# Kernel tuning notes

Hardware: AMD Instinct MI355X
Metric: run time of the kernel (lower is better)

Reference implementation:

```python
import jax, jax.numpy as jnp
import numpy as np
from jax import lax

B, S, P, H = 256, 336, 96, 512


def setup_inputs() -> dict:
    key = jax.random.key(0)
    ks = jax.random.split(key, 18)
    def n(k, shape, s=0.05):
        return jax.random.normal(k, shape, dtype=jnp.float32) * s
    return {
        "x": jax.random.normal(ks[0], (B, S, 7), dtype=jnp.float32),
        "lin_enc_w": n(ks[1], (H, 3)), "lin_enc_b": n(ks[2], (H,)),
        "quat_enc_w": n(ks[3], (H, 4)), "quat_enc_b": n(ks[4], (H,)),
        "lin_wih": n(ks[5], (4 * H, H)), "lin_whh": n(ks[6], (4 * H, H)),
        "lin_bih": n(ks[7], (4 * H,)), "lin_bhh": n(ks[8], (4 * H,)),
        "quat_wih": n(ks[9], (4 * H, H)), "quat_whh": n(ks[10], (4 * H, H)),
        "quat_bih": n(ks[11], (4 * H,)), "quat_bhh": n(ks[12], (4 * H,)),
        "lin_dec_w": n(ks[13], (3, H)), "lin_dec_b": n(ks[14], (3,)),
        "quat_dec_w": n(ks[15], (4, H)), "quat_dec_b": n(ks[16], (4,)),
        "pred_len": P,
    }


def _lstm_cell(carry, xt, Wih, Whh, bih, bhh):
    # PyTorch gate order: i, f, g, o
    h, c = carry
    g = xt @ Wih.T + bih + h @ Whh.T + bhh  # [B, 4H]
    i, f, gg, o = jnp.split(g, 4, axis=-1)
    c = jax.nn.sigmoid(f) * c + jax.nn.sigmoid(i) * jnp.tanh(gg)
    h = jax.nn.sigmoid(o) * jnp.tanh(c)
    return (h, c), h


def _branch(xc, We, be, Wih, Whh, bih, bhh, Wd, bd, pred_len):
    e = xc @ We.T + be  # [B, S, H]
    Bn, _, Hn = e.shape
    cell = lambda carry, xt: _lstm_cell(carry, xt, Wih, Whh, bih, bhh)
    z = jnp.zeros((Bn, Hn), e.dtype)
    (h, _), outs = lax.scan(cell, (z, z), jnp.swapaxes(e, 0, 1))  # outs: [S, B, H]
    # Each prediction step feeds h as input to the LSTM with ZERO initial state
    # (the original code does not pass (h, c) back in).
    def pred_step(h, _):
        (hn, _), _ = cell((jnp.zeros_like(h), jnp.zeros_like(h)), h)
        return hn, hn
    _, preds = lax.scan(pred_step, h, None, length=pred_len)  # [P, B, H]
    seq = jnp.concatenate([outs, preds], axis=0)[1:]  # drop first step -> [S+P-1, B, H]
    return jnp.swapaxes(seq, 0, 1) @ Wd.T + bd


def reference(x, lin_enc_w, lin_enc_b, quat_enc_w, quat_enc_b,
              lin_wih, lin_whh, lin_bih, lin_bhh,
              quat_wih, quat_whh, quat_bih, quat_bhh,
              lin_dec_w, lin_dec_b, quat_dec_w, quat_dec_b, pred_len):
    lx = _branch(x[:, :, :3], lin_enc_w, lin_enc_b, lin_wih, lin_whh,
                 lin_bih, lin_bhh, lin_dec_w, lin_dec_b, pred_len)
    rx = _branch(x[:, :, 3:], quat_enc_w, quat_enc_b, quat_wih, quat_whh,
                 quat_bih, quat_bhh, quat_dec_w, quat_dec_b, pred_len)
    return jnp.concatenate([lx, rx], axis=2)  # [B, S+P-1, 7]
```

## Files before the change

kernel.cpp:

```cpp
#include <hip/hip_runtime.h>

#define BB 256
#define SS 336
#define HH 512
#define NT 431
#define NU 432

typedef __attribute__((ext_vector_type(8))) short bf16x8;
typedef __attribute__((ext_vector_type(16))) float f32x16;
typedef __attribute__((ext_vector_type(4))) int i32x4;


__device__ inline unsigned short f2bf(float f) {
    unsigned int u = __float_as_uint(f);
    unsigned int r = (u + 0x7fffu + ((u >> 16) & 1u)) >> 16;
    return (unsigned short)r;
}
__device__ inline float sigm(float x) { return 1.f / (1.f + __expf(-x)); }
__device__ inline float tanh_(float x) { return 2.f / (1.f + __expf(-2.f * x)) - 1.f; }

__device__ inline i32x4 llc_load_b128(const i32x4* p) {
    i32x4 r;
    asm volatile("global_load_dwordx4 %0, %1, off sc0 sc1" : "=v"(r) : "v"(p));
    return r;
}
__device__ inline void llc_store_b128(i32x4* p, i32x4 v) {
    asm volatile("global_store_dwordx4 %0, %1, off sc0 sc1" :: "v"(p), "v"(v) : "memory");
}
__device__ inline void vm_drain() { asm volatile("s_waitcnt vmcnt(0)" ::: "memory"); }

__global__ void k_wfrag(const float* __restrict__ w0, const float* __restrict__ w1,
                        const float* __restrict__ w2, const float* __restrict__ w3,
                        unsigned short* __restrict__ wfrag) {
    int idx = blockIdx.x * 256 + threadIdx.x;
    int mat = idx >> 17;
    int t = idx & 131071;
    int lane = t & 63;
    int kb = (t >> 6) & 31;
    int csub = (t >> 11) & 1;
    int cg = t >> 12;
    const float* W = mat == 0 ? w0 : (mat == 1 ? w1 : (mat == 2 ? w2 : w3));
    int n_local = csub * 32 + (lane & 31);
    int n = (n_local >> 4) * 512 + cg * 16 + (n_local & 15);
    int k0 = kb * 16 + (lane >> 5) * 8;
    const float* src = W + n * 512 + k0;
    unsigned short us[8];
#pragma unroll
    for (int j = 0; j < 8; ++j) us[j] = f2bf(src[j]);
    i32x4 v;
    v.x = us[0] | (us[1] << 16); v.y = us[2] | (us[3] << 16);
    v.z = us[4] | (us[5] << 16); v.w = us[6] | (us[7] << 16);
    ((i32x4*)wfrag)[idx] = v;
}

__global__ void k_mbias(const float* __restrict__ lin_wih, const float* __restrict__ quat_wih,
                        const float* __restrict__ lin_enc_w, const float* __restrict__ quat_enc_w,
                        const float* __restrict__ lin_enc_b, const float* __restrict__ quat_enc_b,
                        const float* __restrict__ lin_bih, const float* __restrict__ lin_bhh,
                        const float* __restrict__ quat_bih, const float* __restrict__ quat_bhh,
                        float* __restrict__ M, float* __restrict__ bE, float* __restrict__ bP) {
    int gid = blockIdx.x * 256 + threadIdx.x;
    int branch = gid >> 11;
    int n = gid & 2047;
    int nf = 3 + branch;
    const float* Wih = branch ? quat_wih : lin_wih;
    const float* We  = branch ? quat_enc_w : lin_enc_w;
    const float* be  = branch ? quat_enc_b : lin_enc_b;
    const float* bih = branch ? quat_bih : lin_bih;
    const float* bhh = branch ? quat_bhh : lin_bhh;
    float m[4] = {0.f, 0.f, 0.f, 0.f};
    float bs = 0.f;
    for (int j = 0; j < 512; ++j) {
        float w = Wih[n * 512 + j];
#pragma unroll
        for (int kf = 0; kf < 4; ++kf)
            if (kf < nf) m[kf] += w * We[j * nf + kf];
        bs += w * be[j];
    }
    float* Mp = M + (branch * 2048 + n) * 4;
#pragma unroll
    for (int kf = 0; kf < 4; ++kf) Mp[kf] = m[kf];
    bE[branch * 2048 + n] = bs + bih[n] + bhh[n];
    bP[branch * 2048 + n] = bih[n] + bhh[n];
}

__global__ void k_zero(i32x4* __restrict__ p) {
    int idx = blockIdx.x * 256 + threadIdx.x;
    p[idx] = i32x4{0, 0, 0, 0};
}

__global__ __launch_bounds__(256, 1) void k_persist(
    const float* __restrict__ x,
    const unsigned short* __restrict__ wfrag,
    const float* __restrict__ M, const float* __restrict__ bE, const float* __restrict__ bP,
    const float* __restrict__ lin_dec_w, const float* __restrict__ quat_dec_w,
    const float* __restrict__ lin_dec_b, const float* __restrict__ quat_dec_b,
    unsigned short* __restrict__ hbuf,
    float* __restrict__ out,
    unsigned int* __restrict__ bar) {
    __shared__ i32x4 lds_a[4096];
    __shared__ float g_lds[64 * 65];
    __shared__ float h_tile[64 * 17];
    __shared__ float mE[256];
    __shared__ float bEs[64];
    __shared__ float bPs[64];

    const int tid = threadIdx.x;
    const int lane = tid & 63;
    const int wv = tid >> 6;
    const int rsub = wv & 1, csub = wv >> 1;
    const int blk = blockIdx.x;
    const int branch = blk >> 7;
    const int rg = (blk >> 5) & 3;
    const int cg = blk & 31;
    const int group = blk >> 5;
    const int nf = 3 + branch;
    const int row = tid & 63;
    const int jbase = tid >> 6;
    const int b = rg * 64 + row;

    {
        int gate = tid >> 6, jj = (tid >> 2) & 15, kf = tid & 3;
        mE[tid] = M[(size_t)(branch * 2048 + gate * 512 + cg * 16 + jj) * 4 + kf];
    }
    if (tid < 64) {
        int gate = tid >> 4, jj = tid & 15;
        bEs[tid] = bE[branch * 2048 + gate * 512 + cg * 16 + jj];
        bPs[tid] = bP[branch * 2048 + gate * 512 + cg * 16 + jj];
    }

    const int dr   = lane & 1;
    const int dd   = (lane >> 1) & 3;
    const int dseg = lane >> 3;
    const int drow = cg * 2 + dr;
    const bool dvalid = dd < nf;
    const float* dwp = (branch ? quat_dec_w : lin_dec_w) + dd * 512;
    const float dbias = dvalid ? (branch ? quat_dec_b : lin_dec_b)[dd] : 0.f;

    const i32x4* BpE = (const i32x4*)wfrag + (size_t)(branch * 2) * 131072
                       + ((cg * 2 + csub) * 32) * 64 + lane;
    const i32x4* BpP = BpE + 131072;
    i32x4 bw[32];
#pragma unroll
    for (int kb = 0; kb < 32; ++kb) bw[kb] = BpE[kb * 64];

    float creg[4] = {0.f, 0.f, 0.f, 0.f};
    unsigned int* myslot = bar + (size_t)((group << 5) | cg) * 16;

    __syncthreads();

    for (int u = 0; u <= NU; ++u) {
        const int is_enc = (u < SS);

        float xv0 = 0.f, xv1 = 0.f, xv2 = 0.f, xv3 = 0.f;
        if (is_enc) {
            const float* xp = x + ((size_t)b * SS + u) * 7 + branch * 3;
            xv0 = xp[0]; xv1 = xp[1]; xv2 = xp[2];
            if (branch) xv3 = xp[3];
        }
        if (u == SS) {
#pragma unroll
            for (int kb = 0; kb < 32; ++kb) bw[kb] = BpP[kb * 64];
        }

        if (u > 0) {
            if (tid < 64) {
                unsigned int* slot = bar + (size_t)((group << 5) | (lane & 31)) * 16;
                while (!__all((int)(__hip_atomic_load(slot, __ATOMIC_RELAXED,
                                                      __HIP_MEMORY_SCOPE_AGENT)
                                    >= (unsigned int)u)))
                    __builtin_amdgcn_s_sleep(2);
            }
            __syncthreads();
        }

        {
            const i32x4* gsrc = (const i32x4*)hbuf + (size_t)(u & 1) * 32768
                                + (size_t)branch * 16384 + rg * 4096 + tid;
            i32x4 av[16];
#pragma unroll
            for (int i = 0; i < 16; ++i) av[i] = llc_load_b128(gsrc + i * 256);
            vm_drain();
            __builtin_amdgcn_sched_barrier(0);
#pragma unroll
            for (int i = 0; i < 16; ++i) lds_a[i * 256 + tid] = av[i];
        }
        __syncthreads();

        if (u == NU) {
            if (wv == 0) {
                float s = 0.f;
                if (dvalid) {
                    const unsigned short* hp = (const unsigned short*)lds_a;
                    int rowb = (drow >> 5) * 16384 + (drow & 31) * 8;
#pragma unroll
                    for (int jj = 0; jj < 64; ++jj) {
                        int j = dseg * 64 + jj;
                        unsigned short hu = hp[rowb + (j >> 4) * 512 + ((j >> 3) & 1) * 256 + (j & 7)];
                        s += __uint_as_float(((unsigned int)hu) << 16) * dwp[j];
                    }
                }
                s += __shfl_xor(s, 8);
                s += __shfl_xor(s, 16);
                s += __shfl_xor(s, 32);
                if (dseg == 0 && dvalid)
                    out[((size_t)(rg * 64 + drow) * NT + (u - 2)) * 7 + branch * 3 + dd] = s + dbias;
            }
            break;
        }

        f32x16 acc0 = {};
        f32x16 acc1 = {};
        const i32x4* Afrag = lds_a + rsub * 2048 + lane;
#pragma unroll
        for (int kb = 0; kb < 32; kb += 2) {
            i32x4 a0 = Afrag[kb * 64];
            i32x4 a1 = Afrag[(kb + 1) * 64];
            acc0 = __builtin_amdgcn_mfma_f32_32x32x16_bf16(*(const bf16x8*)&a0, *(const bf16x8*)&bw[kb], acc0, 0, 0, 0);
            acc1 = __builtin_amdgcn_mfma_f32_32x32x16_bf16(*(const bf16x8*)&a1, *(const bf16x8*)&bw[kb + 1], acc1, 0, 0, 0);
        }
        int col_l = csub * 32 + (lane & 31);
        int rbase = rsub * 32 + 4 * (lane >> 5);
#pragma unroll
        for (int r = 0; r < 16; ++r) {
            int row_l = rbase + (r & 3) + 8 * (r >> 2);
            g_lds[row_l * 65 + col_l] = acc0[r] + acc1[r];
        }
        __syncthreads();

#pragma unroll
        for (int p = 0; p < 4; ++p) {
            int jj = jbase * 4 + p;
            float gi = g_lds[row * 65 + jj];
            float gf = g_lds[row * 65 + 16 + jj];
            float gc = g_lds[row * 65 + 32 + jj];
            float go = g_lds[row * 65 + 48 + jj];
            if (is_enc) {
                int j4 = jj * 4;
                gi += bEs[jj]      + xv0 * mE[j4]       + xv1 * mE[j4 + 1]       + xv2 * mE[j4 + 2]       + xv3 * mE[j4 + 3];
                gf += bEs[16 + jj] + xv0 * mE[64 + j4]  + xv1 * mE[64 + j4 + 1]  + xv2 * mE[64 + j4 + 2]  + xv3 * mE[64 + j4 + 3];
                gc += bEs[32 + jj] + xv0 * mE[128 + j4] + xv1 * mE[128 + j4 + 1] + xv2 * mE[128 + j4 + 2] + xv3 * mE[128 + j4 + 3];
                go += bEs[48 + jj] + xv0 * mE[192 + j4] + xv1 * mE[192 + j4 + 1] + xv2 * mE[192 + j4 + 2] + xv3 * mE[192 + j4 + 3];
            } else {
                gi += bPs[jj];
                gf += bPs[16 + jj];
                gc += bPs[32 + jj];
                go += bPs[48 + jj];
            }
            float iv = sigm(gi), fv = sigm(gf), gv = tanh_(gc), ov = sigm(go);
            float cn;
            if (is_enc) {
                cn = fv * creg[p] + iv * gv;
                creg[p] = cn;
            } else {
                cn = iv * gv;
            }
            h_tile[row * 17 + jj] = ov * tanh_(cn);
        }
        __syncthreads();

        if (tid < 128) {
            int chunk = tid >> 6;
            int l = tid & 63;
            int row_l = chunk * 32 + (l & 31);
            int jh = (l >> 5) * 8;
            unsigned short us[8];
#pragma unroll
            for (int j = 0; j < 8; ++j) us[j] = f2bf(h_tile[row_l * 17 + jh + j]);
            i32x4 v;
            v.x = us[0] | (us[1] << 16); v.y = us[2] | (us[3] << 16);
            v.z = us[4] | (us[5] << 16); v.w = us[6] | (us[7] << 16);
            int rb = rg * 2 + chunk;
            llc_store_b128((i32x4*)hbuf + (size_t)((u + 1) & 1) * 32768
                           + (size_t)branch * 16384 + (rb * 32 + cg) * 64 + l, v);
        }
        vm_drain();
        __syncthreads();

        if (tid == 0)
            __hip_atomic_store(myslot, (unsigned int)(u + 1), __ATOMIC_RELAXED,
                               __HIP_MEMORY_SCOPE_AGENT);

        if (u >= 2 && wv == 0) {
            float s = 0.f;
            if (dvalid) {
                const unsigned short* hp = (const unsigned short*)lds_a;
                int rowb = (drow >> 5) * 16384 + (drow & 31) * 8;
#pragma unroll
                for (int jj = 0; jj < 64; ++jj) {
                    int j = dseg * 64 + jj;
                    unsigned short hu = hp[rowb + (j >> 4) * 512 + ((j >> 3) & 1) * 256 + (j & 7)];
                    s += __uint_as_float(((unsigned int)hu) << 16) * dwp[j];
                }
            }
            s += __shfl_xor(s, 8);
            s += __shfl_xor(s, 16);
            s += __shfl_xor(s, 32);
            if (dseg == 0 && dvalid)
                out[((size_t)(rg * 64 + drow) * NT + (u - 2)) * 7 + branch * 3 + dd] = s + dbias;
        }
    }
}

extern "C" void kernel_launch(void* const* d_in, const int* in_sizes, int n_in,
                              void* d_out, int out_size, void* d_ws, size_t ws_size,
                              hipStream_t stream) {
    const float* x          = (const float*)d_in[0];
    const float* lin_enc_w  = (const float*)d_in[1];
    const float* lin_enc_b  = (const float*)d_in[2];
    const float* quat_enc_w = (const float*)d_in[3];
    const float* quat_enc_b = (const float*)d_in[4];
    const float* lin_wih    = (const float*)d_in[5];
    const float* lin_whh    = (const float*)d_in[6];
    const float* lin_bih    = (const float*)d_in[7];
    const float* lin_bhh    = (const float*)d_in[8];
    const float* quat_wih   = (const float*)d_in[9];
    const float* quat_whh   = (const float*)d_in[10];
    const float* quat_bih   = (const float*)d_in[11];
    const float* quat_bhh   = (const float*)d_in[12];
    const float* lin_dec_w  = (const float*)d_in[13];
    const float* lin_dec_b  = (const float*)d_in[14];
    const float* quat_dec_w = (const float*)d_in[15];
    const float* quat_dec_b = (const float*)d_in[16];
    float* out = (float*)d_out;
    char* ws = (char*)d_ws;

    unsigned short* wfrag = (unsigned short*)(ws + 0);
    unsigned short* hbuf  = (unsigned short*)(ws + 8388608ull);
    unsigned int*   bar   = (unsigned int*)(ws + 9437184ull);
    float* M    = (float*)(ws + 10485760ull);
    float* bE   = (float*)(ws + 10551296ull);
    float* bP   = (float*)(ws + 10567680ull);

    k_wfrag<<<2048, 256, 0, stream>>>(lin_whh, lin_wih, quat_whh, quat_wih, wfrag);
    k_mbias<<<16, 256, 0, stream>>>(lin_wih, quat_wih, lin_enc_w, quat_enc_w,
                                    lin_enc_b, quat_enc_b, lin_bih, lin_bhh,
                                    quat_bih, quat_bhh, M, bE, bP);
    k_zero<<<260, 256, 0, stream>>>((i32x4*)(ws + 8388608ull));

    k_persist<<<256, 256, 0, stream>>>(x, wfrag, M, bE, bP, lin_dec_w, quat_dec_w,
                                       lin_dec_b, quat_dec_b, hbuf, out, bar);
}
```

Measured before the change: 3.592 ms.

## Retile persistent LSTM to 32-row by 128-column blocks with lighter barrier

Changes the per-block tile from 64 batch rows by 64 gate columns to 32 rows by 128 columns, so each wave owns a full 32-column MFMA tile with one accumulator chain. Sync groups shrink from 32 to 16 blocks. The weight fragment layout is reordered to match. The h-state LDS buffer is double-buffered so the store and flag write can skip a block-wide barrier, and the decoder runs on a different wave that overlaps with the store. The aim is to halve the per-step global h reads per block and cut barrier fan-in, at the cost of a longer serial MFMA chain per wave.

```diff
diff --git a/kernel.cpp b/kernel.cpp
--- a/kernel.cpp
+++ b/kernel.cpp
@@ -37,11 +37,10 @@
     int t = idx & 131071;
     int lane = t & 63;
     int kb = (t >> 6) & 31;
-    int csub = (t >> 11) & 1;
-    int cg = t >> 12;
+    int wq = (t >> 11) & 3;
+    int cg = t >> 13;
     const float* W = mat == 0 ? w0 : (mat == 1 ? w1 : (mat == 2 ? w2 : w3));
-    int n_local = csub * 32 + (lane & 31);
-    int n = (n_local >> 4) * 512 + cg * 16 + (n_local & 15);
+    int n = wq * 512 + cg * 32 + (lane & 31);
     int k0 = kb * 16 + (lane >> 5) * 8;
     const float* src = W + n * 512 + k0;
     unsigned short us[8];
@@ -98,35 +97,34 @@
     unsigned short* __restrict__ hbuf,
     float* __restrict__ out,
     unsigned int* __restrict__ bar) {
-    __shared__ i32x4 lds_a[4096];
-    __shared__ float g_lds[64 * 65];
-    __shared__ float h_tile[64 * 17];
-    __shared__ float mE[256];
-    __shared__ float bEs[64];
-    __shared__ float bPs[64];
+    __shared__ i32x4 lds_a[2][2048];
+    __shared__ float g_lds[32 * 132];
+    __shared__ float h_tile[32 * 33];
+    __shared__ float mE[512];
+    __shared__ float bEs[128];
+    __shared__ float bPs[128];
 
     const int tid = threadIdx.x;
     const int lane = tid & 63;
     const int wv = tid >> 6;
-    const int rsub = wv & 1, csub = wv >> 1;
     const int blk = blockIdx.x;
     const int branch = blk >> 7;
-    const int rg = (blk >> 5) & 3;
-    const int cg = blk & 31;
-    const int group = blk >> 5;
+    const int rg = (blk >> 4) & 7;
+    const int cg = blk & 15;
+    const int group = blk >> 4;
     const int nf = 3 + branch;
-    const int row = tid & 63;
-    const int jbase = tid >> 6;
-    const int b = rg * 64 + row;
-
-    {
-        int gate = tid >> 6, jj = (tid >> 2) & 15, kf = tid & 3;
-        mE[tid] = M[(size_t)(branch * 2048 + gate * 512 + cg * 16 + jj) * 4 + kf];
+    const int row = tid & 31;
+    const int jbase = tid >> 5;
+    const int b = rg * 32 + row;
+
+    for (int t = tid; t < 512; t += 256) {
+        int gate = t >> 7, jj = (t >> 2) & 31, kf = t & 3;
+        mE[t] = M[(size_t)(branch * 2048 + gate * 512 + cg * 32 + jj) * 4 + kf];
     }
-    if (tid < 64) {
-        int gate = tid >> 4, jj = tid & 15;
-        bEs[tid] = bE[branch * 2048 + gate * 512 + cg * 16 + jj];
-        bPs[tid] = bP[branch * 2048 + gate * 512 + cg * 16 + jj];
+    if (tid < 128) {
+        int gate = tid >> 5, jj = tid & 31;
+        bEs[tid] = bE[branch * 2048 + gate * 512 + cg * 32 + jj];
+        bPs[tid] = bP[branch * 2048 + gate * 512 + cg * 32 + jj];
     }
 
     const int dr   = lane & 1;
@@ -138,14 +136,14 @@
     const float dbias = dvalid ? (branch ? quat_dec_b : lin_dec_b)[dd] : 0.f;
 
     const i32x4* BpE = (const i32x4*)wfrag + (size_t)(branch * 2) * 131072
-                       + ((cg * 2 + csub) * 32) * 64 + lane;
+                       + ((cg * 4 + wv) * 32) * 64 + lane;
     const i32x4* BpP = BpE + 131072;
     i32x4 bw[32];
 #pragma unroll
     for (int kb = 0; kb < 32; ++kb) bw[kb] = BpE[kb * 64];
 
     float creg[4] = {0.f, 0.f, 0.f, 0.f};
-    unsigned int* myslot = bar + (size_t)((group << 5) | cg) * 16;
+    unsigned int* myslot = bar + (size_t)blk * 16;
 
     __syncthreads();
 
@@ -164,39 +162,42 @@
         }
 
         if (u > 0) {
-            if (tid < 64) {
-                unsigned int* slot = bar + (size_t)((group << 5) | (lane & 31)) * 16;
-                while (!__all((int)(__hip_atomic_load(slot, __ATOMIC_RELAXED,
-                                                      __HIP_MEMORY_SCOPE_AGENT)
-                                    >= (unsigned int)u)))
-                    __builtin_amdgcn_s_sleep(2);
+            if (wv == 0) {
+                const unsigned int* slot = bar + (size_t)((group << 4) | (lane & 15)) * 16;
+                for (;;) {
+                    unsigned int v;
+                    asm volatile("global_load_dword %0, %1, off sc0 sc1\n\ts_waitcnt vmcnt(0)"
+                                 : "=v"(v) : "v"(slot) : "memory");
+                    if (__all((int)(v >= (unsigned int)u))) break;
+                    __builtin_amdgcn_s_sleep(1);
+                }
             }
             __syncthreads();
         }
 
+        i32x4* lds_cur = lds_a[u & 1];
         {
             const i32x4* gsrc = (const i32x4*)hbuf + (size_t)(u & 1) * 32768
-                                + (size_t)branch * 16384 + rg * 4096 + tid;
-            i32x4 av[16];
-#pragma unroll
-            for (int i = 0; i < 16; ++i) av[i] = llc_load_b128(gsrc + i * 256);
+                                + (size_t)branch * 16384 + rg * 2048 + tid;
+            i32x4 av[8];
+#pragma unroll
+            for (int i = 0; i < 8; ++i) av[i] = llc_load_b128(gsrc + i * 256);
             vm_drain();
             __builtin_amdgcn_sched_barrier(0);
 #pragma unroll
-            for (int i = 0; i < 16; ++i) lds_a[i * 256 + tid] = av[i];
+            for (int i = 0; i < 8; ++i) lds_cur[i * 256 + tid] = av[i];
         }
         __syncthreads();
 
         if (u == NU) {
-            if (wv == 0) {
+            if (wv == 3) {
                 float s = 0.f;
                 if (dvalid) {
-                    const unsigned short* hp = (const unsigned short*)lds_a;
-                    int rowb = (drow >> 5) * 16384 + (drow & 31) * 8;
+                    const unsigned short* hp = (const unsigned short*)lds_cur;
 #pragma unroll
                     for (int jj = 0; jj < 64; ++jj) {
                         int j = dseg * 64 + jj;
-                        unsigned short hu = hp[rowb + (j >> 4) * 512 + ((j >> 3) & 1) * 256 + (j & 7)];
+                        unsigned short hu = hp[(j >> 4) * 512 + ((j >> 3) & 1) * 256 + drow * 8 + (j & 7)];
                         s += __uint_as_float(((unsigned int)hu) << 16) * dwp[j];
                     }
                 }
@@ -204,48 +205,47 @@
                 s += __shfl_xor(s, 16);
                 s += __shfl_xor(s, 32);
                 if (dseg == 0 && dvalid)
-                    out[((size_t)(rg * 64 + drow) * NT + (u - 2)) * 7 + branch * 3 + dd] = s + dbias;
+                    out[((size_t)(rg * 32 + drow) * NT + (u - 2)) * 7 + branch * 3 + dd] = s + dbias;
             }
             break;
         }
 
-        f32x16 acc0 = {};
-        f32x16 acc1 = {};
-        const i32x4* Afrag = lds_a + rsub * 2048 + lane;
-#pragma unroll
-        for (int kb = 0; kb < 32; kb += 2) {
+        f32x16 acc = {};
+        const i32x4* Afrag = lds_cur + lane;
+#pragma unroll
+        for (int kb = 0; kb < 32; ++kb) {
             i32x4 a0 = Afrag[kb * 64];
-            i32x4 a1 = Afrag[(kb + 1) * 64];
-            acc0 = __builtin_amdgcn_mfma_f32_32x32x16_bf16(*(const bf16x8*)&a0, *(const bf16x8*)&bw[kb], acc0, 0, 0, 0);
-            acc1 = __builtin_amdgcn_mfma_f32_32x32x16_bf16(*(const bf16x8*)&a1, *(const bf16x8*)&bw[kb + 1], acc1, 0, 0, 0);
-        }
-        int col_l = csub * 32 + (lane & 31);
-        int rbase = rsub * 32 + 4 * (lane >> 5);
-#pragma unroll
-        for (int r = 0; r < 16; ++r) {
-            int row_l = rbase + (r & 3) + 8 * (r >> 2);
-            g_lds[row_l * 65 + col_l] = acc0[r] + acc1[r];
+            acc = __builtin_amdgcn_mfma_f32_32x32x16_bf16(*(const bf16x8*)&a0, *(const bf16x8*)&bw[kb], acc, 0, 0, 0);
+        }
+        {
+            int col_l = wv * 32 + (lane & 31);
+            int rbase = 4 * (lane >> 5);
+#pragma unroll
+            for (int r = 0; r < 16; ++r) {
+                int row_l = rbase + (r & 3) + 8 * (r >> 2);
+                g_lds[row_l * 132 + col_l] = acc[r];
+            }
         }
         __syncthreads();
 
 #pragma unroll
         for (int p = 0; p < 4; ++p) {
             int jj = jbase * 4 + p;
-            float gi = g_lds[row * 65 + jj];
-            float gf = g_lds[row * 65 + 16 + jj];
-            float gc = g_lds[row * 65 + 32 + jj];
-            float go = g_lds[row * 65 + 48 + jj];
+            float gi = g_lds[row * 132 + jj];
+            float gf = g_lds[row * 132 + 32 + jj];
+            float gc = g_lds[row * 132 + 64 + jj];
+            float go = g_lds[row * 132 + 96 + jj];
             if (is_enc) {
                 int j4 = jj * 4;
                 gi += bEs[jj]      + xv0 * mE[j4]       + xv1 * mE[j4 + 1]       + xv2 * mE[j4 + 2]       + xv3 * mE[j4 + 3];
-                gf += bEs[16 + jj] + xv0 * mE[64 + j4]  + xv1 * mE[64 + j4 + 1]  + xv2 * mE[64 + j4 + 2]  + xv3 * mE[64 + j4 + 3];
-                gc += bEs[32 + jj] + xv0 * mE[128 + j4] + xv1 * mE[128 + j4 + 1] + xv2 * mE[128 + j4 + 2] + xv3 * mE[128 + j4 + 3];
-                go += bEs[48 + jj] + xv0 * mE[192 + j4] + xv1 * mE[192 + j4 + 1] + xv2 * mE[192 + j4 + 2] + xv3 * mE[192 + j4 + 3];
+                gf += bEs[32 + jj] + xv0 * mE[128 + j4] + xv1 * mE[128 + j4 + 1] + xv2 * mE[128 + j4 + 2] + xv3 * mE[128 + j4 + 3];
+                gc += bEs[64 + jj] + xv0 * mE[256 + j4] + xv1 * mE[256 + j4 + 1] + xv2 * mE[256 + j4 + 2] + xv3 * mE[256 + j4 + 3];
+                go += bEs[96 + jj] + xv0 * mE[384 + j4] + xv1 * mE[384 + j4 + 1] + xv2 * mE[384 + j4 + 2] + xv3 * mE[384 + j4 + 3];
             } else {
                 gi += bPs[jj];
-                gf += bPs[16 + jj];
-                gc += bPs[32 + jj];
-                go += bPs[48 + jj];
+                gf += bPs[32 + jj];
+                gc += bPs[64 + jj];
+                go += bPs[96 + jj];
             }
             float iv = sigm(gi), fv = sigm(gf), gv = tanh_(gc), ov = sigm(go);
             float cn;
@@ -255,41 +255,38 @@
             } else {
                 cn = iv * gv;
             }
-            h_tile[row * 17 + jj] = ov * tanh_(cn);
+            h_tile[row * 33 + jj] = ov * tanh_(cn);
         }
         __syncthreads();
 
-        if (tid < 128) {
-            int chunk = tid >> 6;
-            int l = tid & 63;
-            int row_l = chunk * 32 + (l & 31);
-            int jh = (l >> 5) * 8;
-            unsigned short us[8];
-#pragma unroll
-            for (int j = 0; j < 8; ++j) us[j] = f2bf(h_tile[row_l * 17 + jh + j]);
-            i32x4 v;
-            v.x = us[0] | (us[1] << 16); v.y = us[2] | (us[3] << 16);
-            v.z = us[4] | (us[5] << 16); v.w = us[6] | (us[7] << 16);
-            int rb = rg * 2 + chunk;
-            llc_store_b128((i32x4*)hbuf + (size_t)((u + 1) & 1) * 32768
-                           + (size_t)branch * 16384 + (rb * 32 + cg) * 64 + l, v);
-        }
-        vm_drain();
-        __syncthreads();
-
-        if (tid == 0)
-            __hip_atomic_store(myslot, (unsigned int)(u + 1), __ATOMIC_RELAXED,
-                               __HIP_MEMORY_SCOPE_AGENT);
-
-        if (u >= 2 && wv == 0) {
+        if (wv == 0) {
+#pragma unroll
+            for (int chunk = 0; chunk < 2; ++chunk) {
+                int row_l = lane & 31;
+                int ch = chunk * 16 + (lane >> 5) * 8;
+                unsigned short us[8];
+#pragma unroll
+                for (int j = 0; j < 8; ++j) us[j] = f2bf(h_tile[row_l * 33 + ch + j]);
+                i32x4 v;
+                v.x = us[0] | (us[1] << 16); v.y = us[2] | (us[3] << 16);
+                v.z = us[4] | (us[5] << 16); v.w = us[6] | (us[7] << 16);
+                int kb = cg * 2 + chunk;
+                llc_store_b128((i32x4*)hbuf + (size_t)((u + 1) & 1) * 32768
+                               + (size_t)branch * 16384 + rg * 2048 + kb * 64 + lane, v);
+            }
+            vm_drain();
+            if (lane == 0) {
+                unsigned int fl = (unsigned int)(u + 1);
+                asm volatile("global_store_dword %0, %1, off sc0 sc1" :: "v"(myslot), "v"(fl) : "memory");
+            }
+        } else if (wv == 3 && u >= 2) {
             float s = 0.f;
             if (dvalid) {
-                const unsigned short* hp = (const unsigned short*)lds_a;
-                int rowb = (drow >> 5) * 16384 + (drow & 31) * 8;
+                const unsigned short* hp = (const unsigned short*)lds_cur;
 #pragma unroll
                 for (int jj = 0; jj < 64; ++jj) {
                     int j = dseg * 64 + jj;
-                    unsigned short hu = hp[rowb + (j >> 4) * 512 + ((j >> 3) & 1) * 256 + (j & 7)];
+                    unsigned short hu = hp[(j >> 4) * 512 + ((j >> 3) & 1) * 256 + drow * 8 + (j & 7)];
                     s += __uint_as_float(((unsigned int)hu) << 16) * dwp[j];
                 }
             }
@@ -297,7 +294,7 @@
             s += __shfl_xor(s, 16);
             s += __shfl_xor(s, 32);
             if (dseg == 0 && dvalid)
-                out[((size_t)(rg * 64 + drow) * NT + (u - 2)) * 7 + branch * 3 + dd] = s + dbias;
+                out[((size_t)(rg * 32 + drow) * NT + (u - 2)) * 7 + branch * 3 + dd] = s + dbias;
         }
     }
 }
```

Measured after the change: 2.997 ms. 16.6% less time.
